# Performance work log

Measured on AMD Instinct MI355X. Metric: run time of the kernel, lower is better.

Reference implementation:

```python
import jax, jax.numpy as jnp
import numpy as np
from jax import lax

T, B, I, H, FC, O = 2048, 64, 128, 128, 32, 2

def _xavier(key, shape):
    # torch xavier_normal_ on [..., fan_out, fan_in]
    std = float(np.sqrt(2.0 / (shape[-2] + shape[-1])))
    return jax.random.normal(key, shape, jnp.float32) * std

def setup_inputs() -> dict:
    key = jax.random.key(0)
    ks = jax.random.split(key, 16)
    inp = {
        'x': jax.random.normal(ks[0], (T, B, I), jnp.float32),
        'w_ig': _xavier(ks[1], (B, H, I)),
        'w_ii': _xavier(ks[2], (B, H, I)),
        'w_if': _xavier(ks[3], (B, H, I)),
        'w_io': _xavier(ks[4], (B, H, I)),
        'w_hg': _xavier(ks[5], (B, H, H)),
        'w_hi': _xavier(ks[6], (B, H, H)),
        'w_hf': _xavier(ks[7], (B, H, H)),
        'w_ho': _xavier(ks[8], (B, H, H)),
        'b_g': jnp.zeros((B, H, 1), jnp.float32),
        'b_i': jnp.zeros((B, H, 1), jnp.float32),
        'b_f': jnp.zeros((B, H, 1), jnp.float32),
        'b_o': jnp.zeros((B, H, 1), jnp.float32),
        'fc1_w': _xavier(ks[9], (FC, H)),
        'fc1_b': jnp.zeros((FC,), jnp.float32),
        'fc2_w': _xavier(ks[10], (O, FC)),
        'fc2_b': jnp.zeros((O,), jnp.float32),
    }
    return inp

def reference(x, w_ig, w_ii, w_if, w_io, w_hg, w_hi, w_hf, w_ho,
              b_g, b_i, b_f, b_o, fc1_w, fc1_b, fc2_w, fc2_b):
    b, h = w_hg.shape[0], w_hg.shape[1]
    # Original bug: gates read self.hidd which is never updated -> stays zeros.
    hidd0 = jnp.zeros((b, h), x.dtype)
    # Recurrent contributions (identically zero, kept for faithfulness)
    rg = jnp.einsum('bhk,bk->bh', w_hg, hidd0)
    ri = jnp.einsum('bhk,bk->bh', w_hi, hidd0)
    rf = jnp.einsum('bhk,bk->bh', w_hf, hidd0)
    ro = jnp.einsum('bhk,bk->bh', w_ho, hidd0)
    # Input gate pre-activations for all timesteps in one einsum each: [T,B,H]
    g = jnp.tanh(jnp.einsum('bhi,tbi->tbh', w_ig, x) + rg + b_g[:, :, 0])
    i_ = jax.nn.sigmoid(jnp.einsum('bhi,tbi->tbh', w_ii, x) + ri + b_i[:, :, 0])
    f = jax.nn.sigmoid(jnp.einsum('bhi,tbi->tbh', w_if, x) + rf + b_f[:, :, 0])
    o = jax.nn.sigmoid(jnp.einsum('bhi,tbi->tbh', w_io, x) + ro + b_o[:, :, 0])

    def step(carry, gifo):
        c, _ = carry
        g_t, i_t, f_t, o_t = gifo
        c = f_t * c + i_t * g_t
        hid = o_t * jnp.tanh(c)
        return (c, hid), None

    c0 = jnp.zeros((b, h), x.dtype)
    (c_fin, h_fin), _ = lax.scan(step, (c0, c0), (g, i_, f, o))
    # classifier on last hidden: Linear -> tanh -> Linear -> log_softmax
    z = jnp.tanh(h_fin @ fc1_w.T + fc1_b) @ fc2_w.T + fc2_b
    return jax.nn.log_softmax(z, axis=1)
```

## Files before the change

### kernel.cpp

```cpp
#include <hip/hip_runtime.h>
#include <hip/hip_bf16.h>
#include <cstddef>

#define T_DIM 2048
#define B_DIM 64
#define I_DIM 128
#define H_DIM 128
#define FC_DIM 32
#define O_DIM 2

#define NC 16
#define TC (T_DIM / NC)
#define MT 8

#define LOG2E  1.44269504088896f
#define LOG2E2 2.88539008177793f

typedef __attribute__((ext_vector_type(8))) short bf16x8;
typedef __attribute__((ext_vector_type(4))) float f32x4;

__device__ __forceinline__ bf16x8 cvt8(const float* __restrict__ p) {
    union { bf16x8 v; __hip_bfloat162 h2[4]; } u;
#pragma unroll
    for (int j = 0; j < 4; ++j) {
        float2 f2 = {p[2 * j], p[2 * j + 1]};
        u.h2[j] = __float22bfloat162_rn(f2);
    }
    return u.v;
}

__global__ void convert_w_kernel(const float* __restrict__ wg,
                                 const float* __restrict__ wi,
                                 const float* __restrict__ wf,
                                 short* __restrict__ og,
                                 short* __restrict__ oi,
                                 short* __restrict__ of)
{
    const float* src = (blockIdx.y == 0) ? wg : (blockIdx.y == 1) ? wi : wf;
    short* dst       = (blockIdx.y == 0) ? og : (blockIdx.y == 1) ? oi : of;
    const float scale = (blockIdx.y == 0) ? LOG2E2 : LOG2E;
    const size_t idx = ((size_t)blockIdx.x * 256 + threadIdx.x) * 8;
    float4 u0 = *(const float4*)(src + idx);
    float4 u1 = *(const float4*)(src + idx + 4);
    float a[8] = {u0.x * scale, u0.y * scale, u0.z * scale, u0.w * scale,
                  u1.x * scale, u1.y * scale, u1.z * scale, u1.w * scale};
    *(bf16x8*)(dst + idx) = cvt8(a);
}

__global__ __launch_bounds__(512, 4)
void gates_scan_kernel(const float* __restrict__ x,
    const short* __restrict__ wg, const short* __restrict__ wi,
    const short* __restrict__ wf,
    const float* __restrict__ b_g, const float* __restrict__ b_i,
    const float* __restrict__ b_f,
    float* __restrict__ wsF, float* __restrict__ wsA)
{
    __shared__ short frag[MT * 4 * 64 * 8];

    const int L    = threadIdx.x & 63;
    const int wv   = threadIdx.x >> 6;
    const int col  = L & 15;
    const int quad = L >> 4;
    const int bid  = blockIdx.x;
    const int b     = bid & (B_DIM - 1);
    const int chunk = bid >> 6;

    const int h = wv * 16 + col;
    bf16x8 Bg[4], Bi[4], Bf[4];
    {
        const size_t wo = ((size_t)b * H_DIM + h) * I_DIM + quad * 8;
#pragma unroll
        for (int kk = 0; kk < 4; ++kk) {
            Bg[kk] = *(const bf16x8*)(wg + wo + kk * 32);
            Bi[kk] = *(const bf16x8*)(wi + wo + kk * 32);
            Bf[kk] = *(const bf16x8*)(wf + wo + kk * 32);
        }
    }
    const float biasg = b_g[b * H_DIM + h] * LOG2E2;
    const float biasi = b_i[b * H_DIM + h] * LOG2E;
    const float biasf = b_f[b * H_DIM + h] * LOG2E;

    {
        const int mt = wv;
        const int tl = (col >> 2) * 32 + mt * 4 + (col & 3);
        const float* xp = x + ((size_t)(chunk * TC + tl) * B_DIM + b) * I_DIM;
#pragma unroll
        for (int kk = 0; kk < 4; ++kk) {
            const int i0 = quad * 8 + kk * 32;
            float4 u0 = *(const float4*)(xp + i0);
            float4 u1 = *(const float4*)(xp + i0 + 4);
            float a[8] = {u0.x, u0.y, u0.z, u0.w, u1.x, u1.y, u1.z, u1.w};
            *(bf16x8*)(frag + (((mt * 4 + kk) * 64) + L) * 8) = cvt8(a);
        }
    }
    __syncthreads();

    float Fq = 1.0f, Aq = 0.0f;
#pragma unroll 2
    for (int mt = 0; mt < MT; ++mt) {
        bf16x8 ah[4];
#pragma unroll
        for (int kk = 0; kk < 4; ++kk)
            ah[kk] = *(const bf16x8*)(frag + (((mt * 4 + kk) * 64) + L) * 8);
        f32x4 accg = {0.f, 0.f, 0.f, 0.f};
        f32x4 acci = {0.f, 0.f, 0.f, 0.f};
        f32x4 accf = {0.f, 0.f, 0.f, 0.f};
#pragma unroll
        for (int kk = 0; kk < 4; ++kk) {
            accg = __builtin_amdgcn_mfma_f32_16x16x32_bf16(ah[kk], Bg[kk], accg, 0, 0, 0);
            acci = __builtin_amdgcn_mfma_f32_16x16x32_bf16(ah[kk], Bi[kk], acci, 0, 0, 0);
            accf = __builtin_amdgcn_mfma_f32_16x16x32_bf16(ah[kk], Bf[kk], accf, 0, 0, 0);
        }
#pragma unroll
        for (int r = 0; r < 4; ++r) {
            float g  = 2.0f * __builtin_amdgcn_rcpf(
                           1.0f + __builtin_amdgcn_exp2f(-(accg[r] + biasg))) - 1.0f;
            float iv = __builtin_amdgcn_rcpf(
                           1.0f + __builtin_amdgcn_exp2f(-(acci[r] + biasi)));
            float fv = __builtin_amdgcn_rcpf(
                           1.0f + __builtin_amdgcn_exp2f(-(accf[r] + biasf)));
            Aq = fv * Aq + iv * g;
            Fq = fv * Fq;
        }
    }

    float Fo = __shfl_xor(Fq, 16, 64);
    float Ao = __shfl_xor(Aq, 16, 64);
    if ((quad & 1) == 0) { Aq = Fo * Aq + Ao; Fq = Fo * Fq; }
    else                 { Aq = Fq * Ao + Aq; Fq = Fq * Fo; }
    Fo = __shfl_xor(Fq, 32, 64);
    Ao = __shfl_xor(Aq, 32, 64);
    if (quad < 2) { Aq = Fo * Aq + Ao; Fq = Fo * Fq; }
    else          { Aq = Fq * Ao + Aq; Fq = Fq * Fo; }

    if (quad == 0) {
        const int idx = (b * NC + chunk) * H_DIM + h;
        wsF[idx] = Fq;
        wsA[idx] = Aq;
    }
}

__global__ void finish_kernel(const float* __restrict__ x,
    const float* __restrict__ w_io, const float* __restrict__ b_o,
    const float* __restrict__ fc1_w, const float* __restrict__ fc1_b,
    const float* __restrict__ fc2_w, const float* __restrict__ fc2_b,
    const float* __restrict__ wsF, const float* __restrict__ wsA,
    float* __restrict__ out)
{
    const int b = blockIdx.x;
    const int h = threadIdx.x;
    __shared__ float hf[H_DIM];
    __shared__ float z1[FC_DIM];

    float c = 0.0f;
#pragma unroll
    for (int nc = 0; nc < NC; ++nc) {
        const int idx = (b * NC + nc) * H_DIM + h;
        c = wsF[idx] * c + wsA[idx];
    }
    const float* xl = x + ((size_t)(T_DIM - 1) * B_DIM + b) * I_DIM;
    const float* wo = w_io + ((size_t)b * H_DIM + h) * I_DIM;
    float acc = b_o[b * H_DIM + h];
#pragma unroll 8
    for (int i = 0; i < I_DIM; i += 4) {
        float4 xa = *(const float4*)(xl + i);
        float4 wa = *(const float4*)(wo + i);
        acc += xa.x * wa.x + xa.y * wa.y + xa.z * wa.z + xa.w * wa.w;
    }
    const float o = 1.0f / (1.0f + expf(-acc));
    hf[h] = o * tanhf(c);
    __syncthreads();

    if (h < FC_DIM) {
        float a = fc1_b[h];
        const float* w1 = fc1_w + h * H_DIM;
        for (int i = 0; i < H_DIM; ++i) a += w1[i] * hf[i];
        z1[h] = tanhf(a);
    }
    __syncthreads();

    if (h == 0) {
        float z0 = fc2_b[0], zo1 = fc2_b[1];
        for (int j = 0; j < FC_DIM; ++j) {
            z0  += fc2_w[j] * z1[j];
            zo1 += fc2_w[FC_DIM + j] * z1[j];
        }
        const float m = fmaxf(z0, zo1);
        const float lse = m + logf(expf(z0 - m) + expf(zo1 - m));
        out[b * O_DIM + 0] = z0 - lse;
        out[b * O_DIM + 1] = zo1 - lse;
    }
}

extern "C" void kernel_launch(void* const* d_in, const int* in_sizes, int n_in,
                              void* d_out, int out_size, void* d_ws, size_t ws_size,
                              hipStream_t stream) {
    const float* x     = (const float*)d_in[0];
    const float* w_ig  = (const float*)d_in[1];
    const float* w_ii  = (const float*)d_in[2];
    const float* w_if  = (const float*)d_in[3];
    const float* w_io  = (const float*)d_in[4];
    const float* b_g   = (const float*)d_in[9];
    const float* b_i   = (const float*)d_in[10];
    const float* b_f   = (const float*)d_in[11];
    const float* b_o   = (const float*)d_in[12];
    const float* fc1_w = (const float*)d_in[13];
    const float* fc1_b = (const float*)d_in[14];
    const float* fc2_w = (const float*)d_in[15];
    const float* fc2_b = (const float*)d_in[16];

    const size_t NW = (size_t)B_DIM * H_DIM * I_DIM;
    short* wgc = (short*)d_ws;
    short* wic = wgc + NW;
    short* wfc = wic + NW;
    float* wsF = (float*)(wfc + NW);
    float* wsA = wsF + (size_t)B_DIM * NC * H_DIM;
    float* out = (float*)d_out;

    convert_w_kernel<<<dim3(NW / (256 * 8), 3), 256, 0, stream>>>(
        w_ig, w_ii, w_if, wgc, wic, wfc);

    gates_scan_kernel<<<dim3(B_DIM * NC), 512, 0, stream>>>(
        x, wgc, wic, wfc, b_g, b_i, b_f, wsF, wsA);

    finish_kernel<<<B_DIM, 128, 0, stream>>>(x, w_io, b_o, fc1_w, fc1_b,
                                             fc2_w, fc2_b, wsF, wsA, out);
}
```

Baseline: 156.3 us.

## Split time into more chunks, fold negated scale and bias into weights and MFMA accumulator

Raises the number of time chunks from 16 to 64, so each block handles 32 timesteps (2 M-tiles) instead of 128, and the grid grows from 1024 to 4096 blocks. Each thread now loads and converts only one x fragment. The negative log2e scaling is folded into the converted weights and bias, and the bias seeds the MFMA accumulator, which removes per-element negate and add instructions. In exchange the per-block weight register loads are amortized over less work, and the finish kernel now combines 64 partial scan results per sequence instead of 16.

```diff
diff --git a/kernel.cpp b/kernel.cpp
--- a/kernel.cpp
+++ b/kernel.cpp
@@ -9,21 +9,24 @@
 #define FC_DIM 32
 #define O_DIM 2
 
-#define NC 16
+#define NC 64
 #define TC (T_DIM / NC)
-#define MT 8
-
-#define LOG2E  1.44269504088896f
-#define LOG2E2 2.88539008177793f
+#define MT 2
+#define SUBT (TC / 4)
+
+#define NLOG2E  (-1.44269504088896f)
+#define NLOG2E2 (-2.88539008177793f)
 
 typedef __attribute__((ext_vector_type(8))) short bf16x8;
 typedef __attribute__((ext_vector_type(4))) float f32x4;
 
-__device__ __forceinline__ bf16x8 cvt8(const float* __restrict__ p) {
+__device__ __forceinline__ bf16x8 cvt8s(float4 u0, float4 u1, float s) {
     union { bf16x8 v; __hip_bfloat162 h2[4]; } u;
+    float a[8] = {u0.x * s, u0.y * s, u0.z * s, u0.w * s,
+                  u1.x * s, u1.y * s, u1.z * s, u1.w * s};
 #pragma unroll
     for (int j = 0; j < 4; ++j) {
-        float2 f2 = {p[2 * j], p[2 * j + 1]};
+        float2 f2 = {a[2 * j], a[2 * j + 1]};
         u.h2[j] = __float22bfloat162_rn(f2);
     }
     return u.v;
@@ -38,13 +41,11 @@
 {
     const float* src = (blockIdx.y == 0) ? wg : (blockIdx.y == 1) ? wi : wf;
     short* dst       = (blockIdx.y == 0) ? og : (blockIdx.y == 1) ? oi : of;
-    const float scale = (blockIdx.y == 0) ? LOG2E2 : LOG2E;
+    const float scale = (blockIdx.y == 0) ? NLOG2E2 : NLOG2E;
     const size_t idx = ((size_t)blockIdx.x * 256 + threadIdx.x) * 8;
     float4 u0 = *(const float4*)(src + idx);
     float4 u1 = *(const float4*)(src + idx + 4);
-    float a[8] = {u0.x * scale, u0.y * scale, u0.z * scale, u0.w * scale,
-                  u1.x * scale, u1.y * scale, u1.z * scale, u1.w * scale};
-    *(bf16x8*)(dst + idx) = cvt8(a);
+    *(bf16x8*)(dst + idx) = cvt8s(u0, u1, scale);
 }
 
 __global__ __launch_bounds__(512, 4)
@@ -76,35 +77,32 @@
             Bf[kk] = *(const bf16x8*)(wf + wo + kk * 32);
         }
     }
-    const float biasg = b_g[b * H_DIM + h] * LOG2E2;
-    const float biasi = b_i[b * H_DIM + h] * LOG2E;
-    const float biasf = b_f[b * H_DIM + h] * LOG2E;
+    const float biasg = b_g[b * H_DIM + h] * NLOG2E2;
+    const float biasi = b_i[b * H_DIM + h] * NLOG2E;
+    const float biasf = b_f[b * H_DIM + h] * NLOG2E;
 
     {
-        const int mt = wv;
-        const int tl = (col >> 2) * 32 + mt * 4 + (col & 3);
-        const float* xp = x + ((size_t)(chunk * TC + tl) * B_DIM + b) * I_DIM;
-#pragma unroll
-        for (int kk = 0; kk < 4; ++kk) {
-            const int i0 = quad * 8 + kk * 32;
-            float4 u0 = *(const float4*)(xp + i0);
-            float4 u1 = *(const float4*)(xp + i0 + 4);
-            float a[8] = {u0.x, u0.y, u0.z, u0.w, u1.x, u1.y, u1.z, u1.w};
-            *(bf16x8*)(frag + (((mt * 4 + kk) * 64) + L) * 8) = cvt8(a);
-        }
+        const int amt = wv >> 2;
+        const int akk = wv & 3;
+        const int atl = (col >> 2) * SUBT + amt * 4 + (col & 3);
+        const float* xp = x + ((size_t)(chunk * TC + atl) * B_DIM + b) * I_DIM;
+        const int i0 = quad * 8 + akk * 32;
+        float4 u0 = *(const float4*)(xp + i0);
+        float4 u1 = *(const float4*)(xp + i0 + 4);
+        *(bf16x8*)(frag + (((amt * 4 + akk) * 64) + L) * 8) = cvt8s(u0, u1, 1.0f);
     }
     __syncthreads();
 
     float Fq = 1.0f, Aq = 0.0f;
-#pragma unroll 2
+#pragma unroll
     for (int mt = 0; mt < MT; ++mt) {
         bf16x8 ah[4];
 #pragma unroll
         for (int kk = 0; kk < 4; ++kk)
             ah[kk] = *(const bf16x8*)(frag + (((mt * 4 + kk) * 64) + L) * 8);
-        f32x4 accg = {0.f, 0.f, 0.f, 0.f};
-        f32x4 acci = {0.f, 0.f, 0.f, 0.f};
-        f32x4 accf = {0.f, 0.f, 0.f, 0.f};
+        f32x4 accg = {biasg, biasg, biasg, biasg};
+        f32x4 acci = {biasi, biasi, biasi, biasi};
+        f32x4 accf = {biasf, biasf, biasf, biasf};
 #pragma unroll
         for (int kk = 0; kk < 4; ++kk) {
             accg = __builtin_amdgcn_mfma_f32_16x16x32_bf16(ah[kk], Bg[kk], accg, 0, 0, 0);
@@ -113,12 +111,12 @@
         }
 #pragma unroll
         for (int r = 0; r < 4; ++r) {
-            float g  = 2.0f * __builtin_amdgcn_rcpf(
-                           1.0f + __builtin_amdgcn_exp2f(-(accg[r] + biasg))) - 1.0f;
-            float iv = __builtin_amdgcn_rcpf(
-                           1.0f + __builtin_amdgcn_exp2f(-(acci[r] + biasi)));
-            float fv = __builtin_amdgcn_rcpf(
-                           1.0f + __builtin_amdgcn_exp2f(-(accf[r] + biasf)));
+            float eg = __builtin_amdgcn_exp2f(accg[r]);
+            float ei = __builtin_amdgcn_exp2f(acci[r]);
+            float ef = __builtin_amdgcn_exp2f(accf[r]);
+            float g  = 2.0f * __builtin_amdgcn_rcpf(1.0f + eg) - 1.0f;
+            float iv = __builtin_amdgcn_rcpf(1.0f + ei);
+            float fv = __builtin_amdgcn_rcpf(1.0f + ef);
             Aq = fv * Aq + iv * g;
             Fq = fv * Fq;
         }
```

After: 200.6 us. +28.3%, slower.
